# Kernel tuning notes

Hardware: AMD Instinct MI355X
Metric: run time of the kernel (lower is better)

Reference implementation:

```python
import jax, jax.numpy as jnp
import numpy as np

B, L, V, H, NL = 128, 512, 2048, 512, 2


def setup_inputs() -> dict:
    key = jax.random.key(0)
    ks = jax.random.split(key, 20)
    s = 0.05  # param scale
    inp = {
        "input_ids": jax.random.randint(ks[0], (B,), 0, V),
        "last_hidden": jax.random.normal(ks[1], (NL, B, H), jnp.float32),
        "word_dict_vec": jax.random.normal(ks[2], (B, V, H), jnp.float32),
        "encoder_outputs": jax.random.normal(ks[3], (L, B, H), jnp.float32),
        "seq_mask": (jax.random.uniform(ks[4], (B, L)) < 0.2).at[:, 0].set(False),
        # Attn params (torch Linear: y = x @ W.T + b)
        "attn_W": jax.random.normal(ks[5], (H, 2 * H), jnp.float32) * s,
        "attn_b": jax.random.normal(ks[6], (H,), jnp.float32) * s,
        "score_W": jax.random.normal(ks[7], (1, H), jnp.float32) * s,
        # concat layer
        "concat_W": jax.random.normal(ks[8], (H, 2 * H), jnp.float32) * s,
        "concat_b": jax.random.normal(ks[9], (H,), jnp.float32) * s,
        # GRU layer 0 (input 2H) and layer 1 (input H); gates ordered r,z,n as in torch
        "W_ih0": jax.random.normal(ks[10], (3 * H, 2 * H), jnp.float32) * s,
        "W_hh0": jax.random.normal(ks[11], (3 * H, H), jnp.float32) * s,
        "b_ih0": jax.random.normal(ks[12], (3 * H,), jnp.float32) * s,
        "b_hh0": jax.random.normal(ks[13], (3 * H,), jnp.float32) * s,
        "W_ih1": jax.random.normal(ks[14], (3 * H, H), jnp.float32) * s,
        "W_hh1": jax.random.normal(ks[15], (3 * H, H), jnp.float32) * s,
        "b_ih1": jax.random.normal(ks[16], (3 * H,), jnp.float32) * s,
        "b_hh1": jax.random.normal(ks[17], (3 * H,), jnp.float32) * s,
    }
    return inp


def _gru_cell(x, h, W_ih, W_hh, b_ih, b_hh):
    gi = x @ W_ih.T + b_ih
    gh = h @ W_hh.T + b_hh
    i_r, i_z, i_n = jnp.split(gi, 3, axis=-1)
    h_r, h_z, h_n = jnp.split(gh, 3, axis=-1)
    r = jax.nn.sigmoid(i_r + h_r)
    z = jax.nn.sigmoid(i_z + h_z)
    n = jnp.tanh(i_n + r * h_n)
    return (1.0 - z) * n + z * h


def reference(input_ids, last_hidden, word_dict_vec, encoder_outputs, seq_mask,
              attn_W, attn_b, score_W, concat_W, concat_b,
              W_ih0, W_hh0, b_ih0, b_hh0, W_ih1, W_hh1, b_ih1, b_hh1):
    # one_hot @ word_dict_vec == per-batch row gather (same math)
    emb = word_dict_vec[jnp.arange(B), input_ids]  # [B, H]

    # Bahdanau additive attention over encoder_outputs [L, B, H]
    q = last_hidden[-1]  # [B, H]
    hid = jnp.broadcast_to(q[None], (L, B, H))
    energy_in = jnp.concatenate([hid, encoder_outputs], axis=2)  # [L, B, 2H]
    e = jnp.tanh(energy_in @ attn_W.T + attn_b) @ score_W.T      # [L, B, 1]
    scores = e[..., 0].T                                          # [B, L]
    scores = jnp.where(seq_mask, jnp.float32(-1e12), scores)
    aw = jax.nn.softmax(scores, axis=1)                           # [B, L]

    context = jnp.einsum('bl,lbh->bh', aw, encoder_outputs)       # [B, H]

    # single-step 2-layer GRU (eval mode: dropout = identity)
    x0 = jnp.concatenate([emb, context], axis=1)                  # [B, 2H]
    h0 = _gru_cell(x0, last_hidden[0], W_ih0, W_hh0, b_ih0, b_hh0)
    h1 = _gru_cell(h0, last_hidden[1], W_ih1, W_hh1, b_ih1, b_hh1)
    hidden = jnp.stack([h0, h1])                                  # [2, B, H]

    output = jnp.tanh(jnp.concatenate([h1, context], axis=1) @ concat_W.T + concat_b)
    return output, hidden
```

## Files before the change

kernel.cpp:

```cpp
#include <hip/hip_runtime.h>
#include <stdint.h>

#define Hdim 512
#define Bdim 128
#define Ldim 512
#define Vdim 2048

typedef unsigned short u16;
using f32x4  = float  __attribute__((ext_vector_type(4)));
using bf16x8 = __bf16 __attribute__((ext_vector_type(8)));

__device__ inline u16 f2bf(float x) {
  uint32_t u = __float_as_uint(x);
  u += 0x7fffu + ((u >> 16) & 1u);
  return (u16)(u >> 16);
}
__device__ inline uint32_t pk2(float lo, float hi) {
  return (uint32_t)f2bf(lo) | ((uint32_t)f2bf(hi) << 16);
}
__device__ inline float fast_tanh(float x) {
  return 1.0f - 2.0f / (__expf(2.0f * x) + 1.0f);
}
__device__ inline float fast_sig(float x) { return 1.0f / (1.0f + __expf(-x)); }

__device__ inline bf16x8 pack_bf8(float4 x, float4 y) {
  union { uint32_t d[4]; bf16x8 v; } r;
  r.d[0] = pk2(x.x, x.y); r.d[1] = pk2(x.z, x.w);
  r.d[2] = pk2(y.x, y.y); r.d[3] = pk2(y.z, y.w);
  return r.v;
}

__global__ __launch_bounds__(512)
void prep_kernel(const float* __restrict__ lh, const float* __restrict__ attn_W,
                 const float* __restrict__ attn_b, const float* __restrict__ cat_W,
                 const float* __restrict__ W_ih0, const float* __restrict__ W_hh0,
                 const float* __restrict__ W_ih1, const float* __restrict__ W_hh1,
                 const float* __restrict__ b_ih0, const float* __restrict__ b_hh0,
                 const float* __restrict__ b_ih1, const float* __restrict__ b_hh1,
                 const float* __restrict__ wdv, const int* __restrict__ ids,
                 const void* __restrict__ mask,
                 float* __restrict__ qW, u16* __restrict__ arena,
                 float* __restrict__ biasg0, float* __restrict__ biasg1,
                 u16* __restrict__ X0bf, u16* __restrict__ X1bf, int* __restrict__ flag) {
  int blk = blockIdx.x, t = threadIdx.x;
  int lane = t & 63, wid = t >> 6;
  int fr = lane & 15, g = lane >> 4, kof = g * 8;

  if (blk < 16) {
    int mh = wid & 3, nh = wid >> 2;
    int n0 = blk * 32 + nh * 16;
    int rb0 = mh * 32;
    f32x4 ac0 = {0.f, 0.f, 0.f, 0.f}, ac1 = {0.f, 0.f, 0.f, 0.f};
    const float* q = lh + 65536;
#pragma unroll 2
    for (int kt = 0; kt < 512; kt += 32) {
      const float* qr0 = q + (size_t)(rb0 + fr) * 512 + kt + kof;
      const float* qr1 = qr0 + 16 * 512;
      const float* wr  = attn_W + (size_t)(n0 + fr) * 1024 + kt + kof;
      float4 x0 = *(const float4*)qr0, x1 = *(const float4*)(qr0 + 4);
      float4 y0 = *(const float4*)qr1, y1 = *(const float4*)(qr1 + 4);
      float4 w0 = *(const float4*)wr,  w1 = *(const float4*)(wr + 4);
      bf16x8 A0 = pack_bf8(x0, x1), A1 = pack_bf8(y0, y1), Bb = pack_bf8(w0, w1);
      ac0 = __builtin_amdgcn_mfma_f32_16x16x32_bf16(A0, Bb, ac0, 0, 0, 0);
      ac1 = __builtin_amdgcn_mfma_f32_16x16x32_bf16(A1, Bb, ac1, 0, 0, 0);
    }
    float vb = attn_b[n0 + fr];
#pragma unroll
    for (int j = 0; j < 4; ++j) {
      qW[(size_t)(rb0 + g * 4 + j) * 512 + n0 + fr]      = ac0[j] + vb;
      qW[(size_t)(rb0 + 16 + g * 4 + j) * 512 + n0 + fr] = ac1[j] + vb;
    }
    return;
  }
  if (blk == 16) {
    __shared__ int sf;
    if (t == 0) sf = 0;
    __syncthreads();
    const uint32_t* m32 = (const uint32_t*)mask;
    int found = 0;
    for (int i = t; i < 16384; i += 512)
      if (m32[i] & 0xffffff00u) found = 1;
    if (found) sf = 1;
    __syncthreads();
    if (t == 0) *flag = sf;
    return;
  }
  const int ARENA_Q = 1507328;
  int i = (blk - 17) * 512 + t;
  if (i < ARENA_Q) {
    int e = i * 4;
    float4 v = {0.f, 0.f, 0.f, 0.f};
    if (e < 262144) {
      int o = e >> 9, k = e & 511;
      v = *(const float4*)(attn_W + (size_t)o * 1024 + 512 + k);
    } else if (e < 786432) {
      int e2 = e - 262144; int o = e2 >> 10, k = e2 & 1023;
      v = *(const float4*)(cat_W + (size_t)o * 1024 + k);
    } else if (e < 3932160) {
      int e2 = e - 786432; int row = e2 / 1536, k = e2 % 1536;
      int o = row >> 2, gt = row & 3;
      if (gt == 0)      v = (k < 1024) ? *(const float4*)(W_ih0 + (size_t)o * 1024 + k)
                                       : *(const float4*)(W_hh0 + (size_t)o * 512 + k - 1024);
      else if (gt == 1) v = (k < 1024) ? *(const float4*)(W_ih0 + (size_t)(512 + o) * 1024 + k)
                                       : *(const float4*)(W_hh0 + (size_t)(512 + o) * 512 + k - 1024);
      else if (gt == 2) { if (k < 1024)  v = *(const float4*)(W_ih0 + (size_t)(1024 + o) * 1024 + k); }
      else              { if (k >= 1024) v = *(const float4*)(W_hh0 + (size_t)(1024 + o) * 512 + k - 1024); }
    } else {
      int e2 = e - 3932160; int row = e2 >> 10, k = e2 & 1023;
      int o = row >> 2, gt = row & 3;
      if (gt == 0)      v = (k < 512) ? *(const float4*)(W_ih1 + (size_t)o * 512 + k)
                                      : *(const float4*)(W_hh1 + (size_t)o * 512 + k - 512);
      else if (gt == 1) v = (k < 512) ? *(const float4*)(W_ih1 + (size_t)(512 + o) * 512 + k)
                                      : *(const float4*)(W_hh1 + (size_t)(512 + o) * 512 + k - 512);
      else if (gt == 2) { if (k < 512)  v = *(const float4*)(W_ih1 + (size_t)(1024 + o) * 512 + k); }
      else              { if (k >= 512) v = *(const float4*)(W_hh1 + (size_t)(1024 + o) * 512 + k - 512); }
    }
    ushort4 u;
    u.x = f2bf(v.x); u.y = f2bf(v.y); u.z = f2bf(v.z); u.w = f2bf(v.w);
    *(ushort4*)(arena + e) = u;
    return;
  }
  int i2 = i - ARENA_Q;
  if (i2 < 1024) {
    int r4 = i2 * 4; int layer = r4 >> 11; int r = r4 & 2047; int o = r >> 2;
    const float* bi = layer ? b_ih1 : b_ih0;
    const float* bh = layer ? b_hh1 : b_hh0;
    float4 v;
    v.x = bi[o] + bh[o];
    v.y = bi[512 + o] + bh[512 + o];
    v.z = bi[1024 + o];
    v.w = bh[1024 + o];
    *(float4*)((layer ? biasg1 : biasg0) + r) = v;
  } else if (i2 < 1024 + 16384) {
    int j = (i2 - 1024) * 4; int b = j >> 9, i0 = j & 511;
    float4 v = *(const float4*)(wdv + (size_t)b * (Vdim * Hdim) + (size_t)ids[b] * 512 + i0);
    ushort4 u;
    u.x = f2bf(v.x); u.y = f2bf(v.y); u.z = f2bf(v.z); u.w = f2bf(v.w);
    *(ushort4*)(X0bf + b * 1536 + i0) = u;
  } else if (i2 < 1024 + 32768) {
    int j = (i2 - 1024 - 16384) * 4; int b = j >> 9, i0 = j & 511;
    float4 v = *(const float4*)(lh + (size_t)b * 512 + i0);
    ushort4 u;
    u.x = f2bf(v.x); u.y = f2bf(v.y); u.z = f2bf(v.z); u.w = f2bf(v.w);
    *(ushort4*)(X0bf + b * 1536 + 1024 + i0) = u;
  } else if (i2 < 1024 + 49152) {
    int j = (i2 - 1024 - 32768) * 4; int b = j >> 9, i0 = j & 511;
    float4 v = *(const float4*)(lh + 65536 + (size_t)b * 512 + i0);
    ushort4 u;
    u.x = f2bf(v.x); u.y = f2bf(v.y); u.z = f2bf(v.z); u.w = f2bf(v.w);
    *(ushort4*)(X1bf + b * 1024 + 512 + i0) = u;
  }
}

__global__ __launch_bounds__(512)
void attn_kernel(const float* __restrict__ enc, const u16* __restrict__ Wenc,
                 const float* __restrict__ qW, const float* __restrict__ scW,
                 float* __restrict__ scores_p) {
  __shared__ __align__(16) u16 As[2][128 * 40];
  __shared__ float part[8 * 128];
  int blk = blockIdx.x, t = threadIdx.x;
  int lane = t & 63, wid = t >> 6;
  int fr = lane & 15, g = lane >> 4, kof = g * 8;
  int l  = (blk >> 4) * 8 + (blk & 7);
  int oh = (blk >> 3) & 1;
  int ob = oh * 256;
  const int arow = t >> 2;
  const int aks = (t & 3) * 8;

  f32x4 acc[8][2];
#pragma unroll
  for (int i = 0; i < 8; ++i) {
    acc[i][0] = (f32x4){0.f, 0.f, 0.f, 0.f};
    acc[i][1] = (f32x4){0.f, 0.f, 0.f, 0.f};
  }
  const float* abase = enc + ((size_t)l * 128 + arow) * 512 + aks;
  const u16* bptr0 = Wenc + (size_t)(ob + wid * 32 + fr) * 512 + kof;
  const u16* bptr1 = bptr0 + (size_t)16 * 512;

  float4 ra0 = *(const float4*)abase;
  float4 ra1 = *(const float4*)(abase + 4);
  bf16x8 cb0 = *(const bf16x8*)bptr0;
  bf16x8 cb1 = *(const bf16x8*)bptr1;

#pragma unroll 2
  for (int step = 0; step < 16; ++step) {
    int sel = step & 1;
    __syncthreads();
    uint4 ap;
    ap.x = pk2(ra0.x, ra0.y); ap.y = pk2(ra0.z, ra0.w);
    ap.z = pk2(ra1.x, ra1.y); ap.w = pk2(ra1.z, ra1.w);
    *(uint4*)(&As[sel][arow * 40 + aks]) = ap;
    bf16x8 nb0 = cb0, nb1 = cb1;
    if (step < 15) {
      int kt = (step + 1) * 32;
      ra0 = *(const float4*)(abase + kt);
      ra1 = *(const float4*)(abase + kt + 4);
      nb0 = *(const bf16x8*)(bptr0 + kt);
      nb1 = *(const bf16x8*)(bptr1 + kt);
    }
    __syncthreads();
#pragma unroll
    for (int mi = 0; mi < 8; ++mi) {
      bf16x8 av = *(const bf16x8*)(&As[sel][(mi * 16 + fr) * 40 + kof]);
      acc[mi][0] = __builtin_amdgcn_mfma_f32_16x16x32_bf16(av, cb0, acc[mi][0], 0, 0, 0);
      acc[mi][1] = __builtin_amdgcn_mfma_f32_16x16x32_bf16(av, cb1, acc[mi][1], 0, 0, 0);
    }
    cb0 = nb0; cb1 = nb1;
  }
#pragma unroll
  for (int mi = 0; mi < 8; ++mi) {
    float rs0 = 0.f, rs1 = 0.f, rs2 = 0.f, rs3 = 0.f;
#pragma unroll
    for (int ni = 0; ni < 2; ++ni) {
      int o = ob + wid * 32 + ni * 16 + fr;
      float sw = scW[o];
      int brow = mi * 16 + g * 4;
      rs0 += sw * fast_tanh(acc[mi][ni][0] + qW[(size_t)(brow + 0) * 512 + o]);
      rs1 += sw * fast_tanh(acc[mi][ni][1] + qW[(size_t)(brow + 1) * 512 + o]);
      rs2 += sw * fast_tanh(acc[mi][ni][2] + qW[(size_t)(brow + 2) * 512 + o]);
      rs3 += sw * fast_tanh(acc[mi][ni][3] + qW[(size_t)(brow + 3) * 512 + o]);
    }
#pragma unroll
    for (int d = 1; d < 16; d <<= 1) {
      rs0 += __shfl_xor(rs0, d);
      rs1 += __shfl_xor(rs1, d);
      rs2 += __shfl_xor(rs2, d);
      rs3 += __shfl_xor(rs3, d);
    }
    if (fr < 4) {
      float v = (fr == 0) ? rs0 : (fr == 1) ? rs1 : (fr == 2) ? rs2 : rs3;
      part[wid * 128 + mi * 16 + g * 4 + fr] = v;
    }
  }
  __syncthreads();
  if (t < 128) {
    float s = 0.f;
#pragma unroll
    for (int w2 = 0; w2 < 8; ++w2) s += part[w2 * 128 + t];
    scores_p[(size_t)(oh * 128 + t) * 512 + l] = s;
  }
}

__global__ __launch_bounds__(256)
void softctx_kernel(const float* __restrict__ sp, const void* __restrict__ maskp,
                    const int* __restrict__ flag, const float* __restrict__ enc,
                    u16* __restrict__ X0bf, u16* __restrict__ c1bf) {
  __shared__ float wgt[512];
  __shared__ float redm[4], reds[4];
  __shared__ float ps[256 * 2];
  int blk = blockIdx.x, t = threadIdx.x;
  int lane = t & 63, wid = t >> 6;
  int b = blk >> 3, c = blk & 7;
  int l0 = t, l1 = t + 256;
  float s0 = sp[(size_t)b * 512 + l0] + sp[(size_t)(128 + b) * 512 + l0];
  float s1 = sp[(size_t)b * 512 + l1] + sp[(size_t)(128 + b) * 512 + l1];
  bool isbyte = (*flag != 0);
  bool m0, m1;
  if (isbyte) {
    m0 = ((const uint8_t*)maskp)[b * 512 + l0] != 0;
    m1 = ((const uint8_t*)maskp)[b * 512 + l1] != 0;
  } else {
    m0 = ((const int*)maskp)[b * 512 + l0] != 0;
    m1 = ((const int*)maskp)[b * 512 + l1] != 0;
  }
  float v0 = m0 ? -1e12f : s0;
  float v1 = m1 ? -1e12f : s1;
  float mx = fmaxf(v0, v1);
#pragma unroll
  for (int d = 1; d < 64; d <<= 1) mx = fmaxf(mx, __shfl_xor(mx, d));
  if (lane == 0) redm[wid] = mx;
  __syncthreads();
  mx = fmaxf(fmaxf(redm[0], redm[1]), fmaxf(redm[2], redm[3]));
  float e0 = __expf(v0 - mx), e1 = __expf(v1 - mx);
  float sm = e0 + e1;
#pragma unroll
  for (int d = 1; d < 64; d <<= 1) sm += __shfl_xor(sm, d);
  if (lane == 0) reds[wid] = sm;
  __syncthreads();
  sm = reds[0] + reds[1] + reds[2] + reds[3];
  float inv = 1.0f / sm;
  wgt[l0] = e0 * inv;
  wgt[l1] = e1 * inv;
  __syncthreads();
  int cp = t & 31, lq = t >> 5;
  int col = c * 64 + cp * 2;
  float a0 = 0.f, a1 = 0.f;
  const float* ebase = enc + (size_t)b * 512 + col;
#pragma unroll 4
  for (int l2 = lq * 64; l2 < lq * 64 + 64; ++l2) {
    float wl = wgt[l2];
    float2 ev = *(const float2*)(ebase + (size_t)l2 * 65536);
    a0 += wl * ev.x;
    a1 += wl * ev.y;
  }
  ps[(lq * 32 + cp) * 2 + 0] = a0;
  ps[(lq * 32 + cp) * 2 + 1] = a1;
  __syncthreads();
  if (t < 32) {
    float r0 = 0.f, r1 = 0.f;
#pragma unroll
    for (int q2 = 0; q2 < 8; ++q2) {
      r0 += ps[(q2 * 32 + t) * 2 + 0];
      r1 += ps[(q2 * 32 + t) * 2 + 1];
    }
    int cc = c * 64 + t * 2;
    uint32_t packed = pk2(r0, r1);
    *(uint32_t*)(X0bf + b * 1536 + 512 + cc) = packed;
    *(uint32_t*)(c1bf + b * 1024 + 512 + cc) = packed;
  }
}

__global__ __launch_bounds__(256)
void gru_gemm_kernel(const u16* __restrict__ X, int ldx, const u16* __restrict__ Wp,
                     const float* __restrict__ biasp, const float* __restrict__ hprev,
                     int K, float* __restrict__ hout, u16* __restrict__ xdst) {
  __shared__ float ct[128][36];
  int n0 = blockIdx.x * 32;
  int t = threadIdx.x, lane = t & 63, w = t >> 6;
  int fr = lane & 15, g = lane >> 4, kof = g * 8;
  f32x4 acc[2][2];
#pragma unroll
  for (int i = 0; i < 2; ++i)
#pragma unroll
    for (int j = 0; j < 2; ++j) acc[i][j] = (f32x4){0.f, 0.f, 0.f, 0.f};
  const u16* Xr0 = X + (size_t)(w * 32 + fr) * ldx;
  const u16* Xr1 = Xr0 + (size_t)16 * ldx;
  const u16* Wr0 = Wp + (size_t)(n0 + fr) * K;
  const u16* Wr1 = Wp + (size_t)(n0 + 16 + fr) * K;
#pragma unroll 4
  for (int kt = 0; kt < K; kt += 32) {
    bf16x8 a0 = *(const bf16x8*)(Xr0 + kt + kof);
    bf16x8 a1 = *(const bf16x8*)(Xr1 + kt + kof);
    bf16x8 b0 = *(const bf16x8*)(Wr0 + kt + kof);
    bf16x8 b1 = *(const bf16x8*)(Wr1 + kt + kof);
    acc[0][0] = __builtin_amdgcn_mfma_f32_16x16x32_bf16(a0, b0, acc[0][0], 0, 0, 0);
    acc[0][1] = __builtin_amdgcn_mfma_f32_16x16x32_bf16(a0, b1, acc[0][1], 0, 0, 0);
    acc[1][0] = __builtin_amdgcn_mfma_f32_16x16x32_bf16(a1, b0, acc[1][0], 0, 0, 0);
    acc[1][1] = __builtin_amdgcn_mfma_f32_16x16x32_bf16(a1, b1, acc[1][1], 0, 0, 0);
  }
#pragma unroll
  for (int mi = 0; mi < 2; ++mi)
#pragma unroll
    for (int ni = 0; ni < 2; ++ni) {
      int col = ni * 16 + fr;
      float vb = biasp[n0 + col];
#pragma unroll
      for (int j = 0; j < 4; ++j)
        ct[w * 32 + 16 * mi + g * 4 + j][col] = acc[mi][ni][j] + vb;
    }
  __syncthreads();
#pragma unroll
  for (int i = 0; i < 4; ++i) {
    int u = t + i * 256;
    int b = u >> 3, ol = u & 7;
    float cr  = ct[b][ol * 4 + 0];
    float cz  = ct[b][ol * 4 + 1];
    float ci  = ct[b][ol * 4 + 2];
    float chh = ct[b][ol * 4 + 3];
    int o = blockIdx.x * 8 + ol;
    float r = fast_sig(cr), z = fast_sig(cz);
    float n = tanhf(ci + r * chh);
    float h = (1.0f - z) * n + z * hprev[b * 512 + o];
    hout[b * 512 + o] = h;
    xdst[b * 1024 + o] = f2bf(h);
  }
}

__global__ __launch_bounds__(256)
void thin_gemm32(const u16* __restrict__ X, int ldx, const u16* __restrict__ W,
                 const float* __restrict__ bias, float* __restrict__ C, int ldc,
                 int K, int act) {
  int n0 = blockIdx.x * 32;
  int t = threadIdx.x, lane = t & 63, w = t >> 6;
  int fr = lane & 15, g = lane >> 4, kof = g * 8;
  f32x4 acc[2][2];
#pragma unroll
  for (int i = 0; i < 2; ++i)
#pragma unroll
    for (int j = 0; j < 2; ++j) acc[i][j] = (f32x4){0.f, 0.f, 0.f, 0.f};
  const u16* Xr0 = X + (size_t)(w * 32 + fr) * ldx;
  const u16* Xr1 = Xr0 + (size_t)16 * ldx;
  const u16* Wr0 = W + (size_t)(n0 + fr) * K;
  const u16* Wr1 = W + (size_t)(n0 + 16 + fr) * K;
#pragma unroll 4
  for (int kt = 0; kt < K; kt += 32) {
    bf16x8 a0 = *(const bf16x8*)(Xr0 + kt + kof);
    bf16x8 a1 = *(const bf16x8*)(Xr1 + kt + kof);
    bf16x8 b0 = *(const bf16x8*)(Wr0 + kt + kof);
    bf16x8 b1 = *(const bf16x8*)(Wr1 + kt + kof);
    acc[0][0] = __builtin_amdgcn_mfma_f32_16x16x32_bf16(a0, b0, acc[0][0], 0, 0, 0);
    acc[0][1] = __builtin_amdgcn_mfma_f32_16x16x32_bf16(a0, b1, acc[0][1], 0, 0, 0);
    acc[1][0] = __builtin_amdgcn_mfma_f32_16x16x32_bf16(a1, b0, acc[1][0], 0, 0, 0);
    acc[1][1] = __builtin_amdgcn_mfma_f32_16x16x32_bf16(a1, b1, acc[1][1], 0, 0, 0);
  }
#pragma unroll
  for (int mi = 0; mi < 2; ++mi)
#pragma unroll
    for (int ni = 0; ni < 2; ++ni) {
      int col = n0 + ni * 16 + fr;
      float vb = bias[col];
#pragma unroll
      for (int j = 0; j < 4; ++j) {
        int row = w * 32 + 16 * mi + g * 4 + j;
        float v = acc[mi][ni][j] + vb;
        if (act) v = tanhf(v);
        C[(size_t)row * ldc + col] = v;
      }
    }
}

extern "C" void kernel_launch(void* const* d_in, const int* in_sizes, int n_in,
                              void* d_out, int out_size, void* d_ws, size_t ws_size,
                              hipStream_t stream) {
  const int*   ids    = (const int*)  d_in[0];
  const float* lh     = (const float*)d_in[1];
  const float* wdv    = (const float*)d_in[2];
  const float* enc    = (const float*)d_in[3];
  const void*  mask   = d_in[4];
  const float* attn_W = (const float*)d_in[5];
  const float* attn_b = (const float*)d_in[6];
  const float* scW    = (const float*)d_in[7];
  const float* cat_W  = (const float*)d_in[8];
  const float* cat_b  = (const float*)d_in[9];
  const float* W_ih0  = (const float*)d_in[10];
  const float* W_hh0  = (const float*)d_in[11];
  const float* b_ih0  = (const float*)d_in[12];
  const float* b_hh0  = (const float*)d_in[13];
  const float* W_ih1  = (const float*)d_in[14];
  const float* W_hh1  = (const float*)d_in[15];
  const float* b_ih1  = (const float*)d_in[16];
  const float* b_hh1  = (const float*)d_in[17];

  float* out = (float*)d_out;
  float* h0  = out + 65536;
  float* h1  = out + 131072;

  float* ws       = (float*)d_ws;
  float* qW       = ws;
  float* scores_p = ws + 65536;
  float* biasg0   = ws + 196608;
  float* biasg1   = ws + 198656;
  int*   flag     = (int*)(ws + 200704);
  u16*   arena    = (u16*)(ws + 200720);
  u16*   X0bf     = (u16*)(ws + 3215376);
  u16*   X1bf     = (u16*)(ws + 3313680);
  u16*   c1bf     = (u16*)(ws + 3379216);

  const u16* Wenc = arena;
  const u16* Wcat = arena + 262144;
  const u16* Wg0p = arena + 786432;
  const u16* Wg1p = arena + 3932160;

  prep_kernel<<<3059, 512, 0, stream>>>(lh, attn_W, attn_b, cat_W,
                                        W_ih0, W_hh0, W_ih1, W_hh1,
                                        b_ih0, b_hh0, b_ih1, b_hh1,
                                        wdv, ids, mask,
                                        qW, arena, biasg0, biasg1, X0bf, X1bf, flag);
  attn_kernel<<<1024, 512, 0, stream>>>(enc, Wenc, qW, scW, scores_p);
  softctx_kernel<<<1024, 256, 0, stream>>>(scores_p, mask, flag, enc, X0bf, c1bf);
  gru_gemm_kernel<<<64, 256, 0, stream>>>(X0bf, 1536, Wg0p, biasg0, lh, 1536, h0, X1bf);
  gru_gemm_kernel<<<64, 256, 0, stream>>>(X1bf, 1024, Wg1p, biasg1, lh + 65536, 1024, h1, c1bf);
  thin_gemm32<<<16, 256, 0, stream>>>(c1bf, 1024, Wcat, cat_b, out, 512, 1024, 1);
}
```

Baseline: 173.0 us.

## Fuse softmax-context, GRU layers and output GEMM into one cooperative kernel

Replaces the four tail launches (softctx, two GRU GEMMs, final concat GEMM) with a single cooperative kernel of 1024 blocks that uses grid-wide syncs between stages. If the cooperative launch fails, it falls back to separate kernels. It also XOR-swizzles the GRU shared-memory tile to avoid bank conflicts. The goal is to cut launch gaps, at the cost of grid.sync overhead and idle blocks during the small GRU and final stages.

```diff
diff --git a/kernel.cpp b/kernel.cpp
--- a/kernel.cpp
+++ b/kernel.cpp
@@ -1,5 +1,8 @@
 #include <hip/hip_runtime.h>
+#include <hip/hip_cooperative_groups.h>
 #include <stdint.h>
+
+namespace cg = cooperative_groups;
 
 #define Hdim 512
 #define Bdim 128
@@ -241,27 +244,33 @@
   }
 }
 
-__global__ __launch_bounds__(256)
-void softctx_kernel(const float* __restrict__ sp, const void* __restrict__ maskp,
-                    const int* __restrict__ flag, const float* __restrict__ enc,
-                    u16* __restrict__ X0bf, u16* __restrict__ c1bf) {
-  __shared__ float wgt[512];
-  __shared__ float redm[4], reds[4];
-  __shared__ float ps[256 * 2];
-  int blk = blockIdx.x, t = threadIdx.x;
+struct TailArgs {
+  const float* sp; const void* mask; const int* flag; const float* enc;
+  const float* lh;
+  const u16* Wg0p; const u16* Wg1p; const u16* Wcat;
+  const float* biasg0; const float* biasg1; const float* catb;
+  u16* X0bf; u16* X1bf; u16* c1bf;
+  float* h0; float* h1; float* out;
+};
+
+__device__ inline void softctx_body(const TailArgs& a, int blk, int t, float* smem) {
+  float* wgt  = smem;
+  float* redm = wgt + 512;
+  float* reds = redm + 4;
+  float* ps   = smem + 544;
   int lane = t & 63, wid = t >> 6;
   int b = blk >> 3, c = blk & 7;
   int l0 = t, l1 = t + 256;
-  float s0 = sp[(size_t)b * 512 + l0] + sp[(size_t)(128 + b) * 512 + l0];
-  float s1 = sp[(size_t)b * 512 + l1] + sp[(size_t)(128 + b) * 512 + l1];
-  bool isbyte = (*flag != 0);
+  float s0 = a.sp[(size_t)b * 512 + l0] + a.sp[(size_t)(128 + b) * 512 + l0];
+  float s1 = a.sp[(size_t)b * 512 + l1] + a.sp[(size_t)(128 + b) * 512 + l1];
+  bool isbyte = (*a.flag != 0);
   bool m0, m1;
   if (isbyte) {
-    m0 = ((const uint8_t*)maskp)[b * 512 + l0] != 0;
-    m1 = ((const uint8_t*)maskp)[b * 512 + l1] != 0;
+    m0 = ((const uint8_t*)a.mask)[b * 512 + l0] != 0;
+    m1 = ((const uint8_t*)a.mask)[b * 512 + l1] != 0;
   } else {
-    m0 = ((const int*)maskp)[b * 512 + l0] != 0;
-    m1 = ((const int*)maskp)[b * 512 + l1] != 0;
+    m0 = ((const int*)a.mask)[b * 512 + l0] != 0;
+    m1 = ((const int*)a.mask)[b * 512 + l1] != 0;
   }
   float v0 = m0 ? -1e12f : s0;
   float v1 = m1 ? -1e12f : s1;
@@ -285,7 +294,7 @@
   int cp = t & 31, lq = t >> 5;
   int col = c * 64 + cp * 2;
   float a0 = 0.f, a1 = 0.f;
-  const float* ebase = enc + (size_t)b * 512 + col;
+  const float* ebase = a.enc + (size_t)b * 512 + col;
 #pragma unroll 4
   for (int l2 = lq * 64; l2 < lq * 64 + 64; ++l2) {
     float wl = wgt[l2];
@@ -305,19 +314,19 @@
     }
     int cc = c * 64 + t * 2;
     uint32_t packed = pk2(r0, r1);
-    *(uint32_t*)(X0bf + b * 1536 + 512 + cc) = packed;
-    *(uint32_t*)(c1bf + b * 1024 + 512 + cc) = packed;
-  }
-}
-
-__global__ __launch_bounds__(256)
-void gru_gemm_kernel(const u16* __restrict__ X, int ldx, const u16* __restrict__ Wp,
-                     const float* __restrict__ biasp, const float* __restrict__ hprev,
-                     int K, float* __restrict__ hout, u16* __restrict__ xdst) {
-  __shared__ float ct[128][36];
-  int n0 = blockIdx.x * 32;
-  int t = threadIdx.x, lane = t & 63, w = t >> 6;
+    *(uint32_t*)(a.X0bf + b * 1536 + 512 + cc) = packed;
+    *(uint32_t*)(a.c1bf + b * 1024 + 512 + cc) = packed;
+  }
+}
+
+__device__ inline void gru_body(const u16* __restrict__ X, int ldx,
+                                const u16* __restrict__ Wp, const float* __restrict__ biasp,
+                                const float* __restrict__ hprev, int K,
+                                float* __restrict__ hout, u16* __restrict__ xdst,
+                                int blk, int t, float* ct) {
+  int lane = t & 63, w = t >> 6;
   int fr = lane & 15, g = lane >> 4, kof = g * 8;
+  int n0 = blk * 32;
   f32x4 acc[2][2];
 #pragma unroll
   for (int i = 0; i < 2; ++i)
@@ -345,19 +354,22 @@
       int col = ni * 16 + fr;
       float vb = biasp[n0 + col];
 #pragma unroll
-      for (int j = 0; j < 4; ++j)
-        ct[w * 32 + 16 * mi + g * 4 + j][col] = acc[mi][ni][j] + vb;
+      for (int j = 0; j < 4; ++j) {
+        int row = w * 32 + 16 * mi + g * 4 + j;
+        ct[row * 32 + (col ^ ((row & 3) << 3))] = acc[mi][ni][j] + vb;
+      }
     }
   __syncthreads();
 #pragma unroll
   for (int i = 0; i < 4; ++i) {
     int u = t + i * 256;
     int b = u >> 3, ol = u & 7;
-    float cr  = ct[b][ol * 4 + 0];
-    float cz  = ct[b][ol * 4 + 1];
-    float ci  = ct[b][ol * 4 + 2];
-    float chh = ct[b][ol * 4 + 3];
-    int o = blockIdx.x * 8 + ol;
+    int swz = (b & 3) << 3;
+    float cr  = ct[b * 32 + ((ol * 4 + 0) ^ swz)];
+    float cz  = ct[b * 32 + ((ol * 4 + 1) ^ swz)];
+    float ci  = ct[b * 32 + ((ol * 4 + 2) ^ swz)];
+    float chh = ct[b * 32 + ((ol * 4 + 3) ^ swz)];
+    int o = blk * 8 + ol;
     float r = fast_sig(cr), z = fast_sig(cz);
     float n = tanhf(ci + r * chh);
     float h = (1.0f - z) * n + z * hprev[b * 512 + o];
@@ -366,24 +378,21 @@
   }
 }
 
-__global__ __launch_bounds__(256)
-void thin_gemm32(const u16* __restrict__ X, int ldx, const u16* __restrict__ W,
-                 const float* __restrict__ bias, float* __restrict__ C, int ldc,
-                 int K, int act) {
-  int n0 = blockIdx.x * 32;
-  int t = threadIdx.x, lane = t & 63, w = t >> 6;
+__device__ inline void final_body(const TailArgs& a, int blk, int t) {
+  int lane = t & 63, w = t >> 6;
   int fr = lane & 15, g = lane >> 4, kof = g * 8;
+  int n0 = blk * 32;
   f32x4 acc[2][2];
 #pragma unroll
   for (int i = 0; i < 2; ++i)
 #pragma unroll
     for (int j = 0; j < 2; ++j) acc[i][j] = (f32x4){0.f, 0.f, 0.f, 0.f};
-  const u16* Xr0 = X + (size_t)(w * 32 + fr) * ldx;
-  const u16* Xr1 = Xr0 + (size_t)16 * ldx;
-  const u16* Wr0 = W + (size_t)(n0 + fr) * K;
-  const u16* Wr1 = W + (size_t)(n0 + 16 + fr) * K;
+  const u16* Xr0 = a.c1bf + (size_t)(w * 32 + fr) * 1024;
+  const u16* Xr1 = Xr0 + (size_t)16 * 1024;
+  const u16* Wr0 = a.Wcat + (size_t)(n0 + fr) * 1024;
+  const u16* Wr1 = a.Wcat + (size_t)(n0 + 16 + fr) * 1024;
 #pragma unroll 4
-  for (int kt = 0; kt < K; kt += 32) {
+  for (int kt = 0; kt < 1024; kt += 32) {
     bf16x8 a0 = *(const bf16x8*)(Xr0 + kt + kof);
     bf16x8 a1 = *(const bf16x8*)(Xr1 + kt + kof);
     bf16x8 b0 = *(const bf16x8*)(Wr0 + kt + kof);
@@ -398,15 +407,52 @@
 #pragma unroll
     for (int ni = 0; ni < 2; ++ni) {
       int col = n0 + ni * 16 + fr;
-      float vb = bias[col];
+      float vb = a.catb[col];
 #pragma unroll
       for (int j = 0; j < 4; ++j) {
         int row = w * 32 + 16 * mi + g * 4 + j;
-        float v = acc[mi][ni][j] + vb;
-        if (act) v = tanhf(v);
-        C[(size_t)row * ldc + col] = v;
+        a.out[(size_t)row * 512 + col] = tanhf(acc[mi][ni][j] + vb);
       }
     }
+}
+
+__global__ __launch_bounds__(256)
+void tail_coop(TailArgs a) {
+  __shared__ __align__(16) float smem[4096];
+  cg::grid_group gg = cg::this_grid();
+  int blk = blockIdx.x, t = threadIdx.x;
+  softctx_body(a, blk, t, smem);
+  gg.sync();
+  if (blk < 64)
+    gru_body(a.X0bf, 1536, a.Wg0p, a.biasg0, a.lh, 1536, a.h0, a.X1bf, blk, t, smem);
+  gg.sync();
+  if (blk < 64)
+    gru_body(a.X1bf, 1024, a.Wg1p, a.biasg1, a.lh + 65536, 1024, a.h1, a.c1bf, blk, t, smem);
+  gg.sync();
+  if (blk < 16)
+    final_body(a, blk, t);
+}
+
+__global__ __launch_bounds__(256)
+void softctx_k(TailArgs a) {
+  __shared__ __align__(16) float smem[1056];
+  softctx_body(a, blockIdx.x, threadIdx.x, smem);
+}
+__global__ __launch_bounds__(256)
+void gru0_k(TailArgs a) {
+  __shared__ __align__(16) float smem[4096];
+  gru_body(a.X0bf, 1536, a.Wg0p, a.biasg0, a.lh, 1536, a.h0, a.X1bf,
+           blockIdx.x, threadIdx.x, smem);
+}
+__global__ __launch_bounds__(256)
+void gru1_k(TailArgs a) {
+  __shared__ __align__(16) float smem[4096];
+  gru_body(a.X1bf, 1024, a.Wg1p, a.biasg1, a.lh + 65536, 1024, a.h1, a.c1bf,
+           blockIdx.x, threadIdx.x, smem);
+}
+__global__ __launch_bounds__(256)
+void final_k(TailArgs a) {
+  final_body(a, blockIdx.x, threadIdx.x);
 }
 
 extern "C" void kernel_launch(void* const* d_in, const int* in_sizes, int n_in,
@@ -457,8 +503,21 @@
                                         wdv, ids, mask,
                                         qW, arena, biasg0, biasg1, X0bf, X1bf, flag);
   attn_kernel<<<1024, 512, 0, stream>>>(enc, Wenc, qW, scW, scores_p);
-  softctx_kernel<<<1024, 256, 0, stream>>>(scores_p, mask, flag, enc, X0bf, c1bf);
-  gru_gemm_kernel<<<64, 256, 0, stream>>>(X0bf, 1536, Wg0p, biasg0, lh, 1536, h0, X1bf);
-  gru_gemm_kernel<<<64, 256, 0, stream>>>(X1bf, 1024, Wg1p, biasg1, lh + 65536, 1024, h1, c1bf);
-  thin_gemm32<<<16, 256, 0, stream>>>(c1bf, 1024, Wcat, cat_b, out, 512, 1024, 1);
-}
+
+  TailArgs ta;
+  ta.sp = scores_p; ta.mask = mask; ta.flag = flag; ta.enc = enc; ta.lh = lh;
+  ta.Wg0p = Wg0p; ta.Wg1p = Wg1p; ta.Wcat = Wcat;
+  ta.biasg0 = biasg0; ta.biasg1 = biasg1; ta.catb = cat_b;
+  ta.X0bf = X0bf; ta.X1bf = X1bf; ta.c1bf = c1bf;
+  ta.h0 = h0; ta.h1 = h1; ta.out = out;
+  void* params[] = { (void*)&ta };
+  hipError_t err = hipLaunchCooperativeKernel((const void*)tail_coop, dim3(1024),
+                                              dim3(256), params, 0, stream);
+  if (err != hipSuccess) {
+    (void)hipGetLastError();
+    softctx_k<<<1024, 256, 0, stream>>>(ta);
+    gru0_k<<<64, 256, 0, stream>>>(ta);
+    gru1_k<<<64, 256, 0, stream>>>(ta);
+    final_k<<<16, 256, 0, stream>>>(ta);
+  }
+}
```

After: 507.7 us. +193.6%, slower.

## Retile attention GEMM to full output width per block, removing partial score sums

Applied to the files above, without the earlier changes.

The attention-energy GEMM used to split each (l) row block into two halves of the output dimension, each handling all 128 batch rows, and wrote two partial score arrays that softctx then summed. Now each block computes all 512 outputs for 64 batch rows, using a 4x4 MFMA tile per wave, so the score reduction finishes inside the block and the partial buffer goes away. The encoder activations are read once rather than twice, and the extra partial-score traffic disappears. The cost is that each wave now loads four B fragments per step, so the Wenc weights are re-read by both batch-half blocks instead of the encoder rows, and register pressure from 16 accumulators rises.

```diff
diff --git a/kernel.cpp b/kernel.cpp
--- a/kernel.cpp
+++ b/kernel.cpp
@@ -155,66 +155,68 @@
 __global__ __launch_bounds__(512)
 void attn_kernel(const float* __restrict__ enc, const u16* __restrict__ Wenc,
                  const float* __restrict__ qW, const float* __restrict__ scW,
-                 float* __restrict__ scores_p) {
-  __shared__ __align__(16) u16 As[2][128 * 40];
-  __shared__ float part[8 * 128];
+                 float* __restrict__ scores) {
+  __shared__ __align__(16) u16 As[2][64 * 40];
+  __shared__ float part[8 * 64];
   int blk = blockIdx.x, t = threadIdx.x;
   int lane = t & 63, wid = t >> 6;
   int fr = lane & 15, g = lane >> 4, kof = g * 8;
-  int l  = (blk >> 4) * 8 + (blk & 7);
-  int oh = (blk >> 3) & 1;
-  int ob = oh * 256;
-  const int arow = t >> 2;
-  const int aks = (t & 3) * 8;
-
-  f32x4 acc[8][2];
-#pragma unroll
-  for (int i = 0; i < 8; ++i) {
-    acc[i][0] = (f32x4){0.f, 0.f, 0.f, 0.f};
-    acc[i][1] = (f32x4){0.f, 0.f, 0.f, 0.f};
-  }
-  const float* abase = enc + ((size_t)l * 128 + arow) * 512 + aks;
-  const u16* bptr0 = Wenc + (size_t)(ob + wid * 32 + fr) * 512 + kof;
-  const u16* bptr1 = bptr0 + (size_t)16 * 512;
-
-  float4 ra0 = *(const float4*)abase;
-  float4 ra1 = *(const float4*)(abase + 4);
-  bf16x8 cb0 = *(const bf16x8*)bptr0;
-  bf16x8 cb1 = *(const bf16x8*)bptr1;
+  int l  = blk >> 1;
+  int mh = blk & 1;
+  const int arow = t >> 3;
+  const int aseg = (t & 7) * 4;
+
+  f32x4 acc[4][4];
+#pragma unroll
+  for (int i = 0; i < 4; ++i)
+#pragma unroll
+    for (int j = 0; j < 4; ++j) acc[i][j] = (f32x4){0.f, 0.f, 0.f, 0.f};
+
+  const float* abase = enc + ((size_t)l * 128 + mh * 64 + arow) * 512 + aseg;
+  const u16* bbase = Wenc + (size_t)(wid * 64 + fr) * 512 + kof;
+
+  float4 ra = *(const float4*)abase;
+  bf16x8 cb[4];
+#pragma unroll
+  for (int ni = 0; ni < 4; ++ni)
+    cb[ni] = *(const bf16x8*)(bbase + (size_t)(ni * 16) * 512);
 
 #pragma unroll 2
   for (int step = 0; step < 16; ++step) {
     int sel = step & 1;
     __syncthreads();
-    uint4 ap;
-    ap.x = pk2(ra0.x, ra0.y); ap.y = pk2(ra0.z, ra0.w);
-    ap.z = pk2(ra1.x, ra1.y); ap.w = pk2(ra1.z, ra1.w);
-    *(uint4*)(&As[sel][arow * 40 + aks]) = ap;
-    bf16x8 nb0 = cb0, nb1 = cb1;
+    ushort4 ap;
+    ap.x = f2bf(ra.x); ap.y = f2bf(ra.y); ap.z = f2bf(ra.z); ap.w = f2bf(ra.w);
+    *(ushort4*)(&As[sel][arow * 40 + aseg]) = ap;
+    bf16x8 nb[4];
+#pragma unroll
+    for (int ni = 0; ni < 4; ++ni) nb[ni] = cb[ni];
     if (step < 15) {
       int kt = (step + 1) * 32;
-      ra0 = *(const float4*)(abase + kt);
-      ra1 = *(const float4*)(abase + kt + 4);
-      nb0 = *(const bf16x8*)(bptr0 + kt);
-      nb1 = *(const bf16x8*)(bptr1 + kt);
+      ra = *(const float4*)(abase + kt);
+#pragma unroll
+      for (int ni = 0; ni < 4; ++ni)
+        nb[ni] = *(const bf16x8*)(bbase + (size_t)(ni * 16) * 512 + kt);
     }
     __syncthreads();
 #pragma unroll
-    for (int mi = 0; mi < 8; ++mi) {
+    for (int mi = 0; mi < 4; ++mi) {
       bf16x8 av = *(const bf16x8*)(&As[sel][(mi * 16 + fr) * 40 + kof]);
-      acc[mi][0] = __builtin_amdgcn_mfma_f32_16x16x32_bf16(av, cb0, acc[mi][0], 0, 0, 0);
-      acc[mi][1] = __builtin_amdgcn_mfma_f32_16x16x32_bf16(av, cb1, acc[mi][1], 0, 0, 0);
-    }
-    cb0 = nb0; cb1 = nb1;
-  }
-#pragma unroll
-  for (int mi = 0; mi < 8; ++mi) {
+#pragma unroll
+      for (int ni = 0; ni < 4; ++ni)
+        acc[mi][ni] = __builtin_amdgcn_mfma_f32_16x16x32_bf16(av, cb[ni], acc[mi][ni], 0, 0, 0);
+    }
+#pragma unroll
+    for (int ni = 0; ni < 4; ++ni) cb[ni] = nb[ni];
+  }
+#pragma unroll
+  for (int mi = 0; mi < 4; ++mi) {
     float rs0 = 0.f, rs1 = 0.f, rs2 = 0.f, rs3 = 0.f;
 #pragma unroll
-    for (int ni = 0; ni < 2; ++ni) {
-      int o = ob + wid * 32 + ni * 16 + fr;
+    for (int ni = 0; ni < 4; ++ni) {
+      int o = wid * 64 + ni * 16 + fr;
       float sw = scW[o];
-      int brow = mi * 16 + g * 4;
+      int brow = mh * 64 + mi * 16 + g * 4;
       rs0 += sw * fast_tanh(acc[mi][ni][0] + qW[(size_t)(brow + 0) * 512 + o]);
       rs1 += sw * fast_tanh(acc[mi][ni][1] + qW[(size_t)(brow + 1) * 512 + o]);
       rs2 += sw * fast_tanh(acc[mi][ni][2] + qW[(size_t)(brow + 2) * 512 + o]);
@@ -229,20 +231,20 @@
     }
     if (fr < 4) {
       float v = (fr == 0) ? rs0 : (fr == 1) ? rs1 : (fr == 2) ? rs2 : rs3;
-      part[wid * 128 + mi * 16 + g * 4 + fr] = v;
-    }
-  }
-  __syncthreads();
-  if (t < 128) {
+      part[wid * 64 + mi * 16 + g * 4 + fr] = v;
+    }
+  }
+  __syncthreads();
+  if (t < 64) {
     float s = 0.f;
 #pragma unroll
-    for (int w2 = 0; w2 < 8; ++w2) s += part[w2 * 128 + t];
-    scores_p[(size_t)(oh * 128 + t) * 512 + l] = s;
+    for (int w2 = 0; w2 < 8; ++w2) s += part[w2 * 64 + t];
+    scores[(size_t)(mh * 64 + t) * 512 + l] = s;
   }
 }
 
 __global__ __launch_bounds__(256)
-void softctx_kernel(const float* __restrict__ sp, const void* __restrict__ maskp,
+void softctx_kernel(const float* __restrict__ scores, const void* __restrict__ maskp,
                     const int* __restrict__ flag, const float* __restrict__ enc,
                     u16* __restrict__ X0bf, u16* __restrict__ c1bf) {
   __shared__ float wgt[512];
@@ -252,8 +254,8 @@
   int lane = t & 63, wid = t >> 6;
   int b = blk >> 3, c = blk & 7;
   int l0 = t, l1 = t + 256;
-  float s0 = sp[(size_t)b * 512 + l0] + sp[(size_t)(128 + b) * 512 + l0];
-  float s1 = sp[(size_t)b * 512 + l1] + sp[(size_t)(128 + b) * 512 + l1];
+  float s0 = scores[(size_t)b * 512 + l0];
+  float s1 = scores[(size_t)b * 512 + l1];
   bool isbyte = (*flag != 0);
   bool m0, m1;
   if (isbyte) {
@@ -437,14 +439,14 @@
 
   float* ws       = (float*)d_ws;
   float* qW       = ws;
-  float* scores_p = ws + 65536;
-  float* biasg0   = ws + 196608;
-  float* biasg1   = ws + 198656;
-  int*   flag     = (int*)(ws + 200704);
-  u16*   arena    = (u16*)(ws + 200720);
-  u16*   X0bf     = (u16*)(ws + 3215376);
-  u16*   X1bf     = (u16*)(ws + 3313680);
-  u16*   c1bf     = (u16*)(ws + 3379216);
+  float* scores   = ws + 65536;
+  float* biasg0   = ws + 131072;
+  float* biasg1   = ws + 133120;
+  int*   flag     = (int*)(ws + 135168);
+  u16*   arena    = (u16*)(ws + 135184);
+  u16*   X0bf     = (u16*)(ws + 3149840);
+  u16*   X1bf     = (u16*)(ws + 3248144);
+  u16*   c1bf     = (u16*)(ws + 3313680);
 
   const u16* Wenc = arena;
   const u16* Wcat = arena + 262144;
@@ -456,8 +458,8 @@
                                         b_ih0, b_hh0, b_ih1, b_hh1,
                                         wdv, ids, mask,
                                         qW, arena, biasg0, biasg1, X0bf, X1bf, flag);
-  attn_kernel<<<1024, 512, 0, stream>>>(enc, Wenc, qW, scW, scores_p);
-  softctx_kernel<<<1024, 256, 0, stream>>>(scores_p, mask, flag, enc, X0bf, c1bf);
+  attn_kernel<<<1024, 512, 0, stream>>>(enc, Wenc, qW, scW, scores);
+  softctx_kernel<<<1024, 256, 0, stream>>>(scores, mask, flag, enc, X0bf, c1bf);
   gru_gemm_kernel<<<64, 256, 0, stream>>>(X0bf, 1536, Wg0p, biasg0, lh, 1536, h0, X1bf);
   gru_gemm_kernel<<<64, 256, 0, stream>>>(X1bf, 1024, Wg1p, biasg1, lh + 65536, 1024, h1, c1bf);
   thin_gemm32<<<16, 256, 0, stream>>>(c1bf, 1024, Wcat, cat_b, out, 512, 1024, 1);
```

Measured after the change: 186.4 us. 1.08x slower.
